# Kernel tuning notes

Hardware: AMD Instinct MI355X
Metric: run time of the kernel (lower is better)

## Reference

```python
import jax, jax.numpy as jnp
import numpy as np
from jax import lax

# Model config (matches init_kwargs)
SEL = [128, 128]          # radial neighbors per type
A_SEL = [16, 16]          # angular neighbors per type
LAYERS = [256, 256, 256]  # hidden layer sizes, final output dim is 1
N_ATOMS = 4096
N_TYPES = 2
D_DESC = sum(SEL) + 3 * sum(A_SEL)  # 352
BOX = 40.0
EPS = 1e-16


def setup_inputs() -> dict:
    key = jax.random.key(0)
    ks = jax.random.split(key, 16)
    xyz = jax.random.uniform(ks[0], (N_ATOMS, 3), jnp.float32) * BOX
    box_size = jnp.full((3,), BOX, jnp.float32)
    atomtypes = jax.random.randint(ks[1], (N_ATOMS,), 0, N_TYPES, jnp.int32)
    dims = [D_DESC] + LAYERS + [1]
    params = {}
    ki = 2
    for l in range(len(dims) - 1):
        params[f'w{l+1}'] = (jax.random.normal(ks[ki], (N_TYPES, dims[l], dims[l+1]), jnp.float32)
                             / np.sqrt(dims[l]).astype(np.float32))
        params[f'b{l+1}'] = jnp.zeros((N_TYPES, dims[l+1]), jnp.float32)
        ki += 1
    return {'xyz': xyz, 'box_size': box_size, 'atomtypes': atomtypes, **params}


def _descriptors(xyz, box_size, atomtypes):
    """PBC distance matrix + per-type top-k neighbors + DeePMD local-frame descriptor."""
    N = xyz.shape[0]
    # minimum-image displacement (N, N, 3) and distance (N, N)
    dm = xyz[:, None, :] - xyz[None, :, :] + EPS
    dm = dm - box_size * jnp.round(dm / box_size)
    dist = jnp.sqrt(jnp.sum(dm * dm, axis=-1))
    diag = jnp.eye(N, dtype=bool)

    blocks, a_xyz_l, a_dist_l = [], [], []
    lf_dist = lf_idx = None
    for j, selj in enumerate(SEL):
        mask = (atomtypes == j)[None, :] & (~diag)
        dists = jnp.where(mask, dist, jnp.inf)
        # full torch.sort only ever uses the first max(selj, a_selj, 2) columns -> top_k
        k = max(selj, A_SEL[j], 2)
        neg_top, idx = lax.top_k(-dists, k)
        sd = -neg_top  # sorted ascending distances, (N, k)
        if j == 0:
            lf_dist, lf_idx = sd[:, :2], idx[:, :2]
        else:
            cd = jnp.concatenate([lf_dist, sd[:, :2]], axis=1)
            ci = jnp.concatenate([lf_idx, idx[:, :2]], axis=1)
            order = jnp.argsort(cd, axis=1)
            lf_dist = jnp.take_along_axis(cd, order, axis=1)[:, :2]
            lf_idx = jnp.take_along_axis(ci, order, axis=1)[:, :2]
        blocks.append(1.0 / (sd[:, :selj] + EPS))  # inverse-distance radial block
        a_xyz_l.append(jnp.take_along_axis(dm, idx[:, :A_SEL[j], None], axis=1))
        a_dist_l.append(sd[:, :A_SEL[j]])

    a_xyz = jnp.concatenate(a_xyz_l, axis=1)    # (N, sum(a_sel), 3)
    a_dist = jnp.concatenate(a_dist_l, axis=1)  # (N, sum(a_sel))

    # local frame from the two globally nearest neighbors
    l_xyz = jnp.take_along_axis(dm, lf_idx[:, :, None], axis=1) / (lf_dist[:, :, None] + EPS)
    a_n = a_xyz / (a_dist[:, :, None] + EPS)
    r0, r1 = l_xyz[:, 0, :], l_xyz[:, 1, :]
    dot = jnp.sum(r0 * r1, axis=-1, keepdims=True)
    v2 = r1 - dot * r0
    v2 = v2 / jnp.linalg.norm(v2, axis=-1, keepdims=True)
    v3 = jnp.cross(r0, r1)
    v3 = v3 / jnp.linalg.norm(v3, axis=-1, keepdims=True)
    A = jnp.stack([r0, v2, v3], axis=-2)  # (N, 3, 3) rotation to local frame
    rot = jnp.einsum('nij,nkj->nki', A, a_n) / (a_dist[:, :, None] + EPS)  # second 1/r as in source
    return jnp.concatenate(blocks + [rot.reshape(N, 3 * sum(A_SEL))], axis=1)


def reference(xyz, box_size, atomtypes, w1, b1, w2, b2, w3, b3, w4, b4):
    # self.norm is zeros-mean / ones-std -> normalization is the identity
    desc = _descriptors(xyz, box_size, atomtypes)  # (N, D_DESC)
    # evaluate both type-specific MLPs on all atoms, then select per atom type
    h = jnp.tanh(jnp.einsum('nd,tdh->tnh', desc, w1) + b1[:, None, :])
    h = jnp.tanh(jnp.einsum('tnh,thg->tng', h, w2) + b2[:, None, :])
    h = jnp.tanh(jnp.einsum('tng,tgf->tnf', h, w3) + b3[:, None, :])
    out = jnp.einsum('tnf,tfo->tno', h, w4) + b4[:, None, :]  # (T, N, 1)
    energies = out[atomtypes, jnp.arange(desc.shape[0]), 0]
    return jnp.sum(energies)
```

## Files before the change

kernel.cpp:

```cpp
#include <hip/hip_runtime.h>
#include <hip/hip_bf16.h>

#define N_ATOMS 4096
#define NSLAB 32
#define PSTRIDE 8192
#define KSTEPS_TOTAL 27
typedef unsigned long long ull;
typedef __attribute__((ext_vector_type(8))) __bf16 bf16x8;
typedef __attribute__((ext_vector_type(4))) float f32x4;
typedef __attribute__((ext_vector_type(8))) unsigned short u16x8;

__device__ __forceinline__ float wrapr(float d, float box, float rbox) {
    return d - box * rintf(d * rbox);
}

__device__ __forceinline__ float ftanh(float x) {
    float t = __expf(2.0f * x);
    return 1.0f - 2.0f * __builtin_amdgcn_rcpf(t + 1.0f);
}

__global__ __launch_bounds__(256) void prep_kernel(
    const float* __restrict__ xyz, const int* __restrict__ types,
    int* __restrict__ histBlk, float* __restrict__ out,
    const float* __restrict__ w1, const float* __restrict__ w2,
    const float* __restrict__ w3, __hip_bfloat16* __restrict__ Wp)
{
    const int bid = blockIdx.x;
    const int tid = threadIdx.x;
    if (bid < 16) {
        __shared__ int lh[64];
        if (tid < 64) lh[tid] = 0;
        __syncthreads();
        int i = bid * 256 + tid;
        if (i == 0) out[0] = 0.0f;
        int t = types[i];
        int slab = min(NSLAB - 1, (int)(xyz[3*i+2] * (NSLAB / 40.0f)));
        atomicAdd(&lh[t * NSLAB + slab], 1);
        __syncthreads();
        if (tid < 64) histBlk[bid * 64 + tid] = lh[tid];
    } else {
        int idx = (bid - 16) * 256 + tid;
        int n = idx & 255;
        int k = (idx >> 8) % 864;
        int t = idx / (864 * 256);
        int ksg, kr; float v;
        if (k < 352)      { kr = k;       ksg = kr >> 5;        v = w1[((size_t)t*352 + kr)*256 + n]; }
        else if (k < 608) { kr = k - 352; ksg = 11 + (kr >> 5); v = w2[((size_t)t*256 + kr)*256 + n]; }
        else              { kr = k - 608; ksg = 19 + (kr >> 5); v = w3[((size_t)t*256 + kr)*256 + n]; }
        int l  = (((kr & 31) >> 3) << 4) | (n & 15);
        int e  = kr & 7;
        int nt = n >> 4;
        size_t dst = ((((size_t)t*KSTEPS_TOTAL + ksg)*16 + nt) << 9) + (l << 3) + e;
        Wp[dst] = __float2bfloat16(v);
    }
}

__global__ __launch_bounds__(256) void fill_kernel(
    const float* __restrict__ xyz, const int* __restrict__ types,
    const int* __restrict__ histBlk,
    int* __restrict__ slabOffG, int* __restrict__ cntG,
    int* __restrict__ lists, int* __restrict__ posArr,
    float4* __restrict__ packed)
{
    __shared__ int base[64];
    __shared__ int cur[64];
    __shared__ int cntS[2];
    const int tid = threadIdx.x;
    const int bid = blockIdx.x;

    if (tid < 64) {
        int tot = 0, pre = 0;
        #pragma unroll
        for (int b = 0; b < 16; ++b) {
            int h = histBlk[b * 64 + tid];
            tot += h;
            if (b < bid) pre += h;
        }
        int v = tot;
        #pragma unroll
        for (int off = 1; off < 32; off <<= 1) {
            int u = __shfl_up(v, off);
            if ((tid & 31) >= off) v += u;
        }
        base[tid] = (v - tot) + pre;
        cur[tid]  = 0;
        int t = tid >> 5, s = tid & 31;
        if (s == 31) cntS[t] = v;
        if (bid == 0) {
            slabOffG[t * (NSLAB + 1) + s + 1] = v;
            if (s == 0)  slabOffG[t * (NSLAB + 1)] = 0;
            if (s == 31) cntG[t] = v;
        }
    }
    __syncthreads();

    int i = bid * 256 + tid;
    int t = types[i];
    float z = xyz[3*i+2];
    int slab = min(NSLAB - 1, (int)(z * (NSLAB / 40.0f)));
    int ts = t * NSLAB + slab;
    int idx = base[ts] + atomicAdd(&cur[ts], 1);
    lists[t * N_ATOMS + idx] = i;
    posArr[i] = idx;
    float4 pv = make_float4(xyz[3*i+0], xyz[3*i+1], z, __uint_as_float((unsigned)i));
    packed[t * PSTRIDE + idx] = pv;
    packed[t * PSTRIDE + idx + cntS[t]] = pv;
}

__global__ __launch_bounds__(256) void select_kernel(
    const float* __restrict__ xyz, const float* __restrict__ box,
    const int* __restrict__ cnt, const float4* __restrict__ packed,
    const int* __restrict__ slabOffG,
    const int* __restrict__ types, const int* __restrict__ posArr,
    __hip_bfloat16* __restrict__ descB, float* __restrict__ aX,
    float* __restrict__ aD, float* __restrict__ lfD, int* __restrict__ lfJ)
{
    __shared__ ull sortedk[512];
    __shared__ int hist[256];
    __shared__ int basev[256];
    __shared__ int wsum[4];

    const int i   = blockIdx.x >> 1;
    const int t   = blockIdx.x & 1;
    const int tid = threadIdx.x;
    const int n   = cnt[t];
    const float bx = box[0], by = box[1], bz = box[2];
    const float rbx = 1.0f/bx, rby = 1.0f/by, rbz = 1.0f/bz;
    const float xi = xyz[3*i+0], yi = xyz[3*i+1], zi = xyz[3*i+2];
    const unsigned ibits = (unsigned)i;
    const float4* pk = packed + t * PSTRIDE;
    const int* soff = slabOffG + t * (NSLAB + 1);

    float T = __powf(47.75f * bx * by * bz / (float)n, 0.6666667f);
    float Twin = -1.0f, scale = 1.0f;
    int A = 0, L = n;
    int count = 0;
    float d2r[10];

    for (int attempt = 0; attempt < 8; ++attempt) {
        if (T > Twin) {
            float r = sqrtf(T);
            int slo = (int)floorf((zi - r) * (NSLAB / 40.0f)) - 1;
            int shi = (int)floorf((zi + r) * (NSLAB / 40.0f)) + 1;
            int nsl = shi - slo + 1;
            if (nsl >= NSLAB) { A = 0; L = n; }
            else {
                int ss = slo & (NSLAB - 1);
                A = soff[ss];
                int send = ss + nsl;
                L = (send <= NSLAB) ? (soff[send] - A)
                                    : (n - A) + soff[send - NSLAB];
            }
            Twin = T;
            scale = 256.0f / Twin;
            #pragma unroll
            for (int c = 0; c < 10; ++c) {
                d2r[c] = __builtin_inff();
                if ((c << 8) < L) {
                    int m = tid + (c << 8);
                    if (m < L) {
                        float4 p = pk[A + m];
                        if (__float_as_uint(p.w) != ibits) {
                            float ax_ = fabsf(xi - p.x);
                            float ay_ = fabsf(yi - p.y);
                            float az_ = fabsf(zi - p.z);
                            float mx = fminf(ax_, bx - ax_);
                            float my = fminf(ay_, by - ay_);
                            float mz = fminf(az_, bz - az_);
                            d2r[c] = mx*mx + my*my + mz*mz;
                        }
                    }
                }
            }
        }

        hist[tid] = 0;
        __syncthreads();
        #pragma unroll
        for (int c = 0; c < 10; ++c) {
            if (d2r[c] < T)
                atomicAdd(&hist[min(255, (int)(d2r[c] * scale))], 1);
        }
        __syncthreads();
        int h = hist[tid];
        int v = h;
        #pragma unroll
        for (int off = 1; off < 64; off <<= 1) {
            int u = __shfl_up(v, off);
            if ((tid & 63) >= off) v += u;
        }
        if ((tid & 63) == 63) wsum[tid >> 6] = v;
        __syncthreads();
        int woff = 0;
        #pragma unroll
        for (int w2 = 0; w2 < 3; ++w2) if (w2 < (tid >> 6)) woff += wsum[w2];
        basev[tid] = v + woff - h;
        count = wsum[0] + wsum[1] + wsum[2] + wsum[3];
        __syncthreads();
        if (count >= 128 && count <= 511) break;
        T *= (count < 128) ? 1.9f : 0.6f;
    }

    #pragma unroll
    for (int c = 0; c < 10; ++c) {
        if (d2r[c] < T) {
            int b = min(255, (int)(d2r[c] * scale));
            int pp = atomicAdd(&basev[b], 1);
            if (pp < 512) {
                int m = tid + (c << 8);
                unsigned j = __float_as_uint(pk[A + m].w);
                sortedk[pp] = ((ull)__float_as_uint(d2r[c]) << 12) | j;
            }
        }
    }
    __syncthreads();
    const int cnt2 = min(count, 512);

    const int ti = types[i];
    const int pi = posArr[i];
    __hip_bfloat16* drow = descB + ((size_t)ti * N_ATOMS + pi) * 256;
    for (int s = tid; s < cnt2; s += 256) {
        ull k = sortedk[s];
        float d2 = __uint_as_float((unsigned)(k >> 12));
        int b = min(255, (int)(d2 * scale));
        int hh = hist[b];
        int r = s;
        if (hh > 1) {
            int bs = basev[b] - hh;
            int hi2 = min(bs + hh, cnt2);
            r = bs;
            for (int x = bs; x < hi2; ++x) r += (sortedk[x] < k) ? 1 : 0;
        }
        if (r < 128) {
            int j = (int)(k & 0xFFF);
            float dist = sqrtf(d2);
            drow[t * 128 + r] = __float2bfloat16(1.0f / (dist + 1e-16f));
            if (r < 16) {
                float dx = wrapr(xi - xyz[3*j+0], bx, rbx);
                float dy = wrapr(yi - xyz[3*j+1], by, rby);
                float dz = wrapr(zi - xyz[3*j+2], bz, rbz);
                int s2 = i * 32 + t * 16 + r;
                aX[3*s2+0] = dx; aX[3*s2+1] = dy; aX[3*s2+2] = dz;
                aD[s2] = dist;
            }
            if (r < 2) {
                lfD[i * 4 + t * 2 + r] = dist;
                lfJ[i * 4 + t * 2 + r] = j;
            }
        }
    }
}

__global__ __launch_bounds__(256) void mlp_fused_kernel(
    const int* __restrict__ cnt, const int* __restrict__ lists,
    const float* __restrict__ xyz, const float* __restrict__ box,
    const float* __restrict__ aX, const float* __restrict__ aD,
    const float* __restrict__ lfD, const int* __restrict__ lfJ,
    const __hip_bfloat16* __restrict__ descB,
    const __hip_bfloat16* __restrict__ Wp,
    const float* __restrict__ b1, const float* __restrict__ b2,
    const float* __restrict__ b3,
    const float* __restrict__ w4, const float* __restrict__ b4,
    float* __restrict__ out)
{
    __shared__ __hip_bfloat16 Dld[16 * 360];
    __shared__ __hip_bfloat16 Hld[16 * 264];
    __shared__ float b1s[256], b2s[256], b3s[256], w4s[256];
    __shared__ float red[4][16];
    __shared__ float Am[8][12];
    __shared__ int atoms[8];

    const int t   = blockIdx.y;
    const int n_t = cnt[t];
    const int p0  = blockIdx.x * 8;
    if (p0 >= n_t) return;
    const int nv  = min(8, n_t - p0);
    const int tid = threadIdx.x;
    const int w   = tid >> 6;
    const int l   = tid & 63;
    const int lane15 = l & 15;
    const float bx = box[0], by = box[1], bz = box[2];
    const float rbx = 1.0f/bx, rby = 1.0f/by, rbz = 1.0f/bz;

    b1s[tid] = b1[t * 256 + tid];
    b2s[tid] = b2[t * 256 + tid];
    b3s[tid] = b3[t * 256 + tid];
    w4s[tid] = w4[t * 256 + tid];
    if (tid < 8)
        atoms[tid] = (tid < nv) ? lists[t * N_ATOMS + p0 + tid] : -1;

    for (int c = tid; c < 16 * 44; c += 256) {
        int row = c / 44, kc = c - row * 44;
        u16x8 v = {0,0,0,0,0,0,0,0};
        if (row < nv && kc < 32)
            v = *(const u16x8*)&descB[((size_t)t*N_ATOMS + p0 + row)*256 + kc*8];
        *(u16x8*)&Dld[row * 360 + kc * 8] = v;
    }
    __syncthreads();

    if (tid < 8 && atoms[tid] >= 0) {
        const int a = atoms[tid];
        const float xi = xyz[3*a+0], yi = xyz[3*a+1], zi = xyz[3*a+2];
        float cd[4]; int cj[4];
        #pragma unroll
        for (int c = 0; c < 4; ++c) { cd[c] = lfD[a*4+c]; cj[c] = lfJ[a*4+c]; }
        int i0 = 0; float bm = cd[0];
        for (int c = 1; c < 4; ++c) if (cd[c] < bm) { bm = cd[c]; i0 = c; }
        int i1 = -1; float b1v = 3.4e38f;
        for (int c = 0; c < 4; ++c) { if (c == i0) continue; if (cd[c] < b1v) { b1v = cd[c]; i1 = c; } }

        int ja = cj[i0], jb = cj[i1];
        float da = cd[i0], db = cd[i1];
        float r0x = wrapr(xi - xyz[3*ja+0], bx, rbx) / (da + 1e-16f);
        float r0y = wrapr(yi - xyz[3*ja+1], by, rby) / (da + 1e-16f);
        float r0z = wrapr(zi - xyz[3*ja+2], bz, rbz) / (da + 1e-16f);
        float r1x = wrapr(xi - xyz[3*jb+0], bx, rbx) / (db + 1e-16f);
        float r1y = wrapr(yi - xyz[3*jb+1], by, rby) / (db + 1e-16f);
        float r1z = wrapr(zi - xyz[3*jb+2], bz, rbz) / (db + 1e-16f);
        float dot = r0x*r1x + r0y*r1y + r0z*r1z;
        float v2x = r1x - dot*r0x, v2y = r1y - dot*r0y, v2z = r1z - dot*r0z;
        float n2 = sqrtf(v2x*v2x + v2y*v2y + v2z*v2z);
        v2x /= n2; v2y /= n2; v2z /= n2;
        float v3x = r0y*r1z - r0z*r1y;
        float v3y = r0z*r1x - r0x*r1z;
        float v3z = r0x*r1y - r0y*r1x;
        float n3 = sqrtf(v3x*v3x + v3y*v3y + v3z*v3z);
        v3x /= n3; v3y /= n3; v3z /= n3;
        Am[tid][0]=r0x; Am[tid][1]=r0y; Am[tid][2]=r0z;
        Am[tid][3]=v2x; Am[tid][4]=v2y; Am[tid][5]=v2z;
        Am[tid][6]=v3x; Am[tid][7]=v3y; Am[tid][8]=v3z;
    }
    __syncthreads();

    if (tid < 128) {
        const int q = tid >> 4, s = tid & 15;
        const int a = atoms[q];
        if (a >= 0) {
            #pragma unroll
            for (int half = 0; half < 2; ++half) {
                int ss = s + (half << 4);
                int sidx = a * 32 + ss;
                float d  = aD[sidx];
                float dn = d + 1e-16f;
                float ax = aX[3*sidx+0] / dn;
                float ay = aX[3*sidx+1] / dn;
                float az = aX[3*sidx+2] / dn;
                float o0 = (Am[q][0]*ax + Am[q][1]*ay + Am[q][2]*az) / dn;
                float o1 = (Am[q][3]*ax + Am[q][4]*ay + Am[q][5]*az) / dn;
                float o2 = (Am[q][6]*ax + Am[q][7]*ay + Am[q][8]*az) / dn;
                Dld[q*360 + 256 + 3*ss + 0] = __float2bfloat16(o0);
                Dld[q*360 + 256 + 3*ss + 1] = __float2bfloat16(o1);
                Dld[q*360 + 256 + 3*ss + 2] = __float2bfloat16(o2);
            }
        }
    }
    __syncthreads();

    const __hip_bfloat16* wpt = Wp + (((size_t)t * KSTEPS_TOTAL * 16 + (w << 2)) << 9);
    const int aoff = ((l >> 4) << 3);
    const int rb   = ((l >> 4) << 2);

    f32x4 acc0 = {0,0,0,0}, acc1 = {0,0,0,0}, acc2 = {0,0,0,0}, acc3 = {0,0,0,0};

#define KSTEP(SRC, STRIDE, KSG) { \
    bf16x8 a = *(const bf16x8*)&SRC[lane15 * STRIDE + (ks << 5) + aoff]; \
    const __hip_bfloat16* wk = wpt + (((size_t)(KSG) << 13)) + (l << 3); \
    bf16x8 bv0 = *(const bf16x8*)(wk); \
    bf16x8 bv1 = *(const bf16x8*)(wk + 512); \
    bf16x8 bv2 = *(const bf16x8*)(wk + 1024); \
    bf16x8 bv3 = *(const bf16x8*)(wk + 1536); \
    acc0 = __builtin_amdgcn_mfma_f32_16x16x32_bf16(a, bv0, acc0, 0, 0, 0); \
    acc1 = __builtin_amdgcn_mfma_f32_16x16x32_bf16(a, bv1, acc1, 0, 0, 0); \
    acc2 = __builtin_amdgcn_mfma_f32_16x16x32_bf16(a, bv2, acc2, 0, 0, 0); \
    acc3 = __builtin_amdgcn_mfma_f32_16x16x32_bf16(a, bv3, acc3, 0, 0, 0); }

#define STORE_H(ACC, NT, DST, STRIDE, BS) if (rb < nv) { \
    int n = (w << 6) + ((NT) << 4) + lane15; \
    float bb = BS[n]; \
    DST[(rb + 0) * STRIDE + n] = __float2bfloat16(ftanh(ACC[0] + bb)); \
    DST[(rb + 1) * STRIDE + n] = __float2bfloat16(ftanh(ACC[1] + bb)); \
    DST[(rb + 2) * STRIDE + n] = __float2bfloat16(ftanh(ACC[2] + bb)); \
    DST[(rb + 3) * STRIDE + n] = __float2bfloat16(ftanh(ACC[3] + bb)); }

    #pragma unroll 2
    for (int ks = 0; ks < 11; ++ks) KSTEP(Dld, 360, ks)
    STORE_H(acc0, 0, Hld, 264, b1s)
    STORE_H(acc1, 1, Hld, 264, b1s)
    STORE_H(acc2, 2, Hld, 264, b1s)
    STORE_H(acc3, 3, Hld, 264, b1s)
    __syncthreads();

    acc0 = (f32x4){0,0,0,0}; acc1 = acc0; acc2 = acc0; acc3 = acc0;
    #pragma unroll 2
    for (int ks = 0; ks < 8; ++ks) KSTEP(Hld, 264, 11 + ks)
    __syncthreads();
    STORE_H(acc0, 0, Dld, 360, b2s)
    STORE_H(acc1, 1, Dld, 360, b2s)
    STORE_H(acc2, 2, Dld, 360, b2s)
    STORE_H(acc3, 3, Dld, 360, b2s)
    __syncthreads();

    acc0 = (f32x4){0,0,0,0}; acc1 = acc0; acc2 = acc0; acc3 = acc0;
    #pragma unroll 2
    for (int ks = 0; ks < 8; ++ks) KSTEP(Dld, 360, 19 + ks)

    float s0 = 0.f, s1 = 0.f, s2 = 0.f, s3 = 0.f;
#define EPART(ACC, NT) if (rb < nv) { \
    int n = (w << 6) + ((NT) << 4) + lane15; \
    float wv = w4s[n]; float bb = b3s[n]; \
    s0 += ftanh(ACC[0] + bb) * wv; s1 += ftanh(ACC[1] + bb) * wv; \
    s2 += ftanh(ACC[2] + bb) * wv; s3 += ftanh(ACC[3] + bb) * wv; }
    EPART(acc0, 0) EPART(acc1, 1) EPART(acc2, 2) EPART(acc3, 3)

    #pragma unroll
    for (int off = 1; off <= 8; off <<= 1) {
        s0 += __shfl_xor(s0, off);
        s1 += __shfl_xor(s1, off);
        s2 += __shfl_xor(s2, off);
        s3 += __shfl_xor(s3, off);
    }
    if (lane15 == 0) {
        red[w][rb + 0] = s0;
        red[w][rb + 1] = s1;
        red[w][rb + 2] = s2;
        red[w][rb + 3] = s3;
    }
    __syncthreads();

    if (tid < 16) {
        float e = red[0][tid] + red[1][tid] + red[2][tid] + red[3][tid];
        e = (tid < nv) ? (e + b4[t]) : 0.0f;
        #pragma unroll
        for (int off = 1; off <= 8; off <<= 1) e += __shfl_xor(e, off);
        if (tid == 0) atomicAdd(out, e);
    }
#undef KSTEP
#undef STORE_H
#undef EPART
}

extern "C" void kernel_launch(void* const* d_in, const int* in_sizes, int n_in,
                              void* d_out, int out_size, void* d_ws, size_t ws_size,
                              hipStream_t stream) {
    const float* xyz   = (const float*)d_in[0];
    const float* box   = (const float*)d_in[1];
    const int*   types = (const int*)  d_in[2];
    const float* w1 = (const float*)d_in[3];
    const float* b1 = (const float*)d_in[4];
    const float* w2 = (const float*)d_in[5];
    const float* b2 = (const float*)d_in[6];
    const float* w3 = (const float*)d_in[7];
    const float* b3 = (const float*)d_in[8];
    const float* w4 = (const float*)d_in[9];
    const float* b4 = (const float*)d_in[10];
    float* out = (float*)d_out;

    float* p = (float*)d_ws;
    int*    histBlk  = (int*)p;        p += 16 * 64;
    int*    cnt      = (int*)p;        p += 16;
    int*    slabOffG = (int*)p;        p += 68;
    int*    posArr   = (int*)p;        p += N_ATOMS;
    int*    lists    = (int*)p;        p += 2 * N_ATOMS;
    p += 4;
    float4* packed   = (float4*)p;     p += 2 * PSTRIDE * 4;
    float*  lfD      = p;              p += 4 * N_ATOMS;
    int*    lfJ      = (int*)p;        p += 4 * N_ATOMS;
    float*  aX       = p;              p += 96 * N_ATOMS;
    float*  aD       = p;              p += 32 * N_ATOMS;
    __hip_bfloat16* descB = (__hip_bfloat16*)p;
    p += (size_t)2 * N_ATOMS * 256 / 2;
    __hip_bfloat16* Wp = (__hip_bfloat16*)p;
    p += (size_t)2 * KSTEPS_TOTAL * 16 * 512 / 2;

    prep_kernel<<<16 + (2 * 864 * 256) / 256, 256, 0, stream>>>(
        xyz, types, histBlk, out, w1, w2, w3, Wp);
    fill_kernel<<<16, 256, 0, stream>>>(xyz, types, histBlk,
                                        slabOffG, cnt, lists, posArr, packed);
    select_kernel<<<2 * N_ATOMS, 256, 0, stream>>>(
        xyz, box, cnt, packed, slabOffG, types, posArr, descB, aX, aD, lfD, lfJ);
    dim3 g(N_ATOMS / 8, 2);
    mlp_fused_kernel<<<g, 256, 0, stream>>>(cnt, lists, xyz, box, aX, aD, lfD, lfJ,
                                            descB, Wp, b1, b2, b3, w4, b4, out);
}
```

Before: 70.31 us.

## Merge histogram and fill kernels by recomputing full histogram per block; tune search radius

The separate prep (histogram) and fill (scatter) kernels are folded into one launch. Each of the 16 binning blocks now recomputes the whole-atom histogram and its own prefix counts redundantly, so no global histogram handoff or second launch is needed. The initial neighbor-search radius heuristic constant is also lowered so the first attempt scans fewer slabs, at the risk of needing more retries when too few candidates are found. The redundant per-block histogram adds some work and shared atomics.

```diff
diff --git a/kernel.cpp b/kernel.cpp
--- a/kernel.cpp
+++ b/kernel.cpp
@@ -19,25 +19,69 @@
     return 1.0f - 2.0f * __builtin_amdgcn_rcpf(t + 1.0f);
 }
 
-__global__ __launch_bounds__(256) void prep_kernel(
+__global__ __launch_bounds__(256) void fill_kernel(
     const float* __restrict__ xyz, const int* __restrict__ types,
-    int* __restrict__ histBlk, float* __restrict__ out,
+    int* __restrict__ slabOffG, int* __restrict__ cntG,
+    int* __restrict__ lists, int* __restrict__ posArr,
+    float4* __restrict__ packed, float* __restrict__ out,
     const float* __restrict__ w1, const float* __restrict__ w2,
     const float* __restrict__ w3, __hip_bfloat16* __restrict__ Wp)
 {
     const int bid = blockIdx.x;
     const int tid = threadIdx.x;
+
     if (bid < 16) {
-        __shared__ int lh[64];
-        if (tid < 64) lh[tid] = 0;
-        __syncthreads();
-        int i = bid * 256 + tid;
-        if (i == 0) out[0] = 0.0f;
+        __shared__ int lhAll[64];
+        __shared__ int lhPre[64];
+        __shared__ int base[64];
+        __shared__ int cur[64];
+        __shared__ int cntS[2];
+
+        if (tid < 64) { lhAll[tid] = 0; lhPre[tid] = 0; cur[tid] = 0; }
+        __syncthreads();
+
+        const int myBase = bid * 256;
+        for (int m = tid; m < N_ATOMS; m += 256) {
+            int t = types[m];
+            int slab = min(NSLAB - 1, (int)(xyz[3*m+2] * (NSLAB / 40.0f)));
+            int ts = t * NSLAB + slab;
+            atomicAdd(&lhAll[ts], 1);
+            if (m < myBase) atomicAdd(&lhPre[ts], 1);
+        }
+        __syncthreads();
+
+        if (tid < 64) {
+            int tot = lhAll[tid];
+            int v = tot;
+            #pragma unroll
+            for (int off = 1; off < 32; off <<= 1) {
+                int u = __shfl_up(v, off);
+                if ((tid & 31) >= off) v += u;
+            }
+            base[tid] = v - tot;
+            int t = tid >> 5, s = tid & 31;
+            if (s == 31) cntS[t] = v;
+            if (bid == 0) {
+                slabOffG[t * (NSLAB + 1) + s + 1] = v;
+                if (s == 0)  slabOffG[t * (NSLAB + 1)] = 0;
+                if (s == 31) cntG[t] = v;
+            }
+        }
+        if (bid == 0 && tid == 0) out[0] = 0.0f;
+        __syncthreads();
+
+        int i = myBase + tid;
         int t = types[i];
-        int slab = min(NSLAB - 1, (int)(xyz[3*i+2] * (NSLAB / 40.0f)));
-        atomicAdd(&lh[t * NSLAB + slab], 1);
-        __syncthreads();
-        if (tid < 64) histBlk[bid * 64 + tid] = lh[tid];
+        float z = xyz[3*i+2];
+        int slab = min(NSLAB - 1, (int)(z * (NSLAB / 40.0f)));
+        int ts = t * NSLAB + slab;
+        int idx = base[ts] + lhPre[ts] + atomicAdd(&cur[ts], 1);
+        lists[t * N_ATOMS + idx] = i;
+        posArr[i] = idx;
+        float4 pv = make_float4(xyz[3*i+0], xyz[3*i+1], z,
+                                __uint_as_float((unsigned)i));
+        packed[t * PSTRIDE + idx] = pv;
+        packed[t * PSTRIDE + idx + cntS[t]] = pv;
     } else {
         int idx = (bid - 16) * 256 + tid;
         int n = idx & 255;
@@ -55,58 +99,6 @@
     }
 }
 
-__global__ __launch_bounds__(256) void fill_kernel(
-    const float* __restrict__ xyz, const int* __restrict__ types,
-    const int* __restrict__ histBlk,
-    int* __restrict__ slabOffG, int* __restrict__ cntG,
-    int* __restrict__ lists, int* __restrict__ posArr,
-    float4* __restrict__ packed)
-{
-    __shared__ int base[64];
-    __shared__ int cur[64];
-    __shared__ int cntS[2];
-    const int tid = threadIdx.x;
-    const int bid = blockIdx.x;
-
-    if (tid < 64) {
-        int tot = 0, pre = 0;
-        #pragma unroll
-        for (int b = 0; b < 16; ++b) {
-            int h = histBlk[b * 64 + tid];
-            tot += h;
-            if (b < bid) pre += h;
-        }
-        int v = tot;
-        #pragma unroll
-        for (int off = 1; off < 32; off <<= 1) {
-            int u = __shfl_up(v, off);
-            if ((tid & 31) >= off) v += u;
-        }
-        base[tid] = (v - tot) + pre;
-        cur[tid]  = 0;
-        int t = tid >> 5, s = tid & 31;
-        if (s == 31) cntS[t] = v;
-        if (bid == 0) {
-            slabOffG[t * (NSLAB + 1) + s + 1] = v;
-            if (s == 0)  slabOffG[t * (NSLAB + 1)] = 0;
-            if (s == 31) cntG[t] = v;
-        }
-    }
-    __syncthreads();
-
-    int i = bid * 256 + tid;
-    int t = types[i];
-    float z = xyz[3*i+2];
-    int slab = min(NSLAB - 1, (int)(z * (NSLAB / 40.0f)));
-    int ts = t * NSLAB + slab;
-    int idx = base[ts] + atomicAdd(&cur[ts], 1);
-    lists[t * N_ATOMS + idx] = i;
-    posArr[i] = idx;
-    float4 pv = make_float4(xyz[3*i+0], xyz[3*i+1], z, __uint_as_float((unsigned)i));
-    packed[t * PSTRIDE + idx] = pv;
-    packed[t * PSTRIDE + idx + cntS[t]] = pv;
-}
-
 __global__ __launch_bounds__(256) void select_kernel(
     const float* __restrict__ xyz, const float* __restrict__ box,
     const int* __restrict__ cnt, const float4* __restrict__ packed,
@@ -131,7 +123,7 @@
     const float4* pk = packed + t * PSTRIDE;
     const int* soff = slabOffG + t * (NSLAB + 1);
 
-    float T = __powf(47.75f * bx * by * bz / (float)n, 0.6666667f);
+    float T = __powf(38.2f * bx * by * bz / (float)n, 0.6666667f);
     float Twin = -1.0f, scale = 1.0f;
     int A = 0, L = n;
     int count = 0;
@@ -456,12 +448,11 @@
     float* out = (float*)d_out;
 
     float* p = (float*)d_ws;
-    int*    histBlk  = (int*)p;        p += 16 * 64;
     int*    cnt      = (int*)p;        p += 16;
     int*    slabOffG = (int*)p;        p += 68;
     int*    posArr   = (int*)p;        p += N_ATOMS;
     int*    lists    = (int*)p;        p += 2 * N_ATOMS;
-    p += 4;
+    p += 12;
     float4* packed   = (float4*)p;     p += 2 * PSTRIDE * 4;
     float*  lfD      = p;              p += 4 * N_ATOMS;
     int*    lfJ      = (int*)p;        p += 4 * N_ATOMS;
@@ -472,10 +463,8 @@
     __hip_bfloat16* Wp = (__hip_bfloat16*)p;
     p += (size_t)2 * KSTEPS_TOTAL * 16 * 512 / 2;
 
-    prep_kernel<<<16 + (2 * 864 * 256) / 256, 256, 0, stream>>>(
-        xyz, types, histBlk, out, w1, w2, w3, Wp);
-    fill_kernel<<<16, 256, 0, stream>>>(xyz, types, histBlk,
-                                        slabOffG, cnt, lists, posArr, packed);
+    fill_kernel<<<16 + (2 * 864 * 256) / 256, 256, 0, stream>>>(
+        xyz, types, slabOffG, cnt, lists, posArr, packed, out, w1, w2, w3, Wp);
     select_kernel<<<2 * N_ATOMS, 256, 0, stream>>>(
         xyz, box, cnt, packed, slabOffG, types, posArr, descB, aX, aD, lfD, lfJ);
     dim3 g(N_ATOMS / 8, 2);
```

After: 67.66 us, median of 2. 3.8% less time.
